# Kernel tuning notes

Measured on AMD Instinct MI355X. Metric: run time of the kernel, lower is better.

The kernel has to match this reference:

```python
import jax, jax.numpy as jnp
import numpy as np


def setup_inputs() -> dict:
    key = jax.random.key(0)
    ks = jax.random.split(key, 8)
    B, N, K, C_in, M, C_add, C_out = 2, 40000, 16, 64, 16, 3, 128
    in_features = (C_in + C_add) * M  # 1072
    input_features = jax.random.normal(ks[0], (B, N, C_in), dtype=jnp.float32)
    neighbor_inds = jax.random.randint(ks[1], (B, N, K), 0, N, dtype=jnp.int64)
    inverse_neighbors = jax.random.randint(ks[2], (B, N * K), 0, N * K, dtype=jnp.int64)
    inverse_k = jax.random.randint(ks[3], (B, N * K), 0, K, dtype=jnp.int64)
    inverse_idx = jax.random.randint(ks[4], (B, N * K), 0, N, dtype=jnp.int64)
    weightnet = jax.random.normal(ks[5], (B, N, K, M), dtype=jnp.float32)
    additional_features = jax.random.normal(ks[6], (B, N, K, C_add), dtype=jnp.float32)
    bound = 1.0 / np.sqrt(in_features)
    kw, kb = jax.random.split(ks[7])
    linear_weight = jax.random.uniform(kw, (C_out, in_features), dtype=jnp.float32, minval=-bound, maxval=bound)
    linear_bias = jax.random.uniform(kb, (C_out,), dtype=jnp.float32, minval=-bound, maxval=bound)
    return {
        "input_features": input_features,
        "neighbor_inds": neighbor_inds,
        "inverse_neighbors": inverse_neighbors,
        "inverse_k": inverse_k,
        "inverse_idx": inverse_idx,
        "weightnet": weightnet,
        "additional_features": additional_features,
        "linear_weight": linear_weight,
        "linear_bias": linear_bias,
    }


def reference(input_features, neighbor_inds, inverse_neighbors, inverse_k, inverse_idx,
              weightnet, additional_features, linear_weight, linear_bias):
    # inverse_* tensors are only used by the custom CUDA backward; unused here.
    B, N, K = neighbor_inds.shape
    # gather neighbor features: [B, N, K, C_in]
    gathered = jnp.take_along_axis(input_features[:, :, None, :],
                                   neighbor_inds[..., None], axis=1)
    # concat extra per-neighbor features -> [B, N, K, C]
    feats = jnp.concatenate([gathered, additional_features], axis=-1)
    # PConv: [B,N,C,K] @ [B,N,K,M] -> [B,N,C,M] -> flatten to [B,N,C*M]
    pconv = jnp.einsum('bnkc,bnkm->bncm', feats, weightnet)
    pconv = pconv.reshape(B, N, -1)
    # fused linear
    out = jnp.einsum('bnf,of->bno', pconv, linear_weight) + linear_bias
    return out
```

## Files before the change

kernel.cpp:

```cpp
#include <hip/hip_runtime.h>
#include <stdint.h>

typedef unsigned short u16;
typedef short short8 __attribute__((ext_vector_type(8)));
typedef float floatx4 __attribute__((ext_vector_type(4)));

#define NPERB   40000
#define NPTS    80000
#define KNBR    16
#define CIN     64
#define MDIM    16
#define CADD    3
#define CF      (CIN + CADD)
#define COUT    128
#define KF      1072
#define KP      1088
#define NKT     34
#define PTSB    16
#define SLAB    65
#define GRB     64
#define PPB     8

__device__ __forceinline__ u16 f2bf(float f) {
    union { float f; unsigned int u; } v; v.f = f;
    unsigned int u = v.u;
    return (u16)((u + 0x7FFFu + ((u >> 16) & 1u)) >> 16);
}
__device__ __forceinline__ short8 pack8(floatx4 x, floatx4 y) {
    union { short8 v; u16 a[8]; } u;
    u.a[0] = f2bf(x[0]); u.a[1] = f2bf(x[1]); u.a[2] = f2bf(x[2]); u.a[3] = f2bf(x[3]);
    u.a[4] = f2bf(y[0]); u.a[5] = f2bf(y[1]); u.a[6] = f2bf(y[2]); u.a[7] = f2bf(y[3]);
    return u.v;
}
__device__ __forceinline__ unsigned swz(unsigned chunk) {
    return chunk ^ ((chunk >> 3) & 7u);
}
__device__ __forceinline__ void gload_lds16(const void* g, void* l) {
    __builtin_amdgcn_global_load_lds(
        (const __attribute__((address_space(1))) void*)g,
        (__attribute__((address_space(3))) void*)l, 16, 0, 0);
}

__global__ void prep_lw_kernel(const float* __restrict__ lw, u16* __restrict__ lwp) {
    int i = blockIdx.x * 256 + threadIdx.x;
    if (i >= COUT * KP) return;
    int o = i / KP, f = i - o * KP;
    lwp[i] = (f < KF) ? f2bf(lw[(size_t)o * KF + f]) : (u16)0;
}

__device__ __forceinline__ void emit_point(
    int lane, float av, const float (&fv)[KNBR], const float* wl,
    u16* __restrict__ dst)
{
    const int em = lane & 15, ec = lane >> 4;
    float ev = 0.f;
#pragma unroll
    for (int k = 0; k < KNBR; k++)
        ev += __shfl(av, k * CADD + ec) * wl[k * MDIM + em];
    if (ec == 3) ev = 0.f;
    dst[1024 + lane] = f2bf(ev);

    floatx4 a0 = 0, a1 = 0, a2 = 0, a3 = 0;
#pragma unroll
    for (int k = 0; k < KNBR; k++) {
        const floatx4* w4 = (const floatx4*)(wl + k * MDIM);
        const float fvk = fv[k];
        a0 += fvk * w4[0]; a1 += fvk * w4[1];
        a2 += fvk * w4[2]; a3 += fvk * w4[3];
    }
    *(short8*)(dst + lane * 16)     = pack8(a0, a1);
    *(short8*)(dst + lane * 16 + 8) = pack8(a2, a3);
}

__global__ __launch_bounds__(256) void pconv_kernel(
    const float* __restrict__ inp,
    const int*   __restrict__ nbr,
    const float* __restrict__ wn,
    const float* __restrict__ addl,
    u16* __restrict__ pc)
{
    __shared__ __align__(16) float Wns[PPB * KNBR * MDIM];

    const int wave = threadIdx.x >> 6;
    const int lane = threadIdx.x & 63;
    const int pbase = blockIdx.x * PPB;
    const float* inpb = inp + ((pbase >= NPERB) ? (size_t)NPERB * CIN : 0);

    const int pr0 = wave * 2;
    const int p0  = __builtin_amdgcn_readfirstlane(pbase + pr0);
    const int p1  = p0 + 1;

    float* wl0 = Wns + pr0 * (KNBR * MDIM);
    float* wl1 = wl0 + KNBR * MDIM;
    gload_lds16(wn + (size_t)p0 * (KNBR * MDIM) + lane * 4, wl0);
    gload_lds16(wn + (size_t)p1 * (KNBR * MDIM) + lane * 4, wl1);

    float av0 = (lane < KNBR * CADD) ? addl[(size_t)p0 * (KNBR * CADD) + lane] : 0.f;
    float av1 = (lane < KNBR * CADD) ? addl[(size_t)p1 * (KNBR * CADD) + lane] : 0.f;

    const int* nb0 = nbr + (size_t)p0 * KNBR;
    const int* nb1 = nbr + (size_t)p1 * KNBR;
    int idx0[KNBR], idx1[KNBR];
#pragma unroll
    for (int k = 0; k < KNBR; k++) idx0[k] = nb0[k];
#pragma unroll
    for (int k = 0; k < KNBR; k++) idx1[k] = nb1[k];

    float fv0[KNBR], fv1[KNBR];
#pragma unroll
    for (int k = 0; k < KNBR; k++) fv0[k] = inpb[(size_t)idx0[k] * CIN + lane];
#pragma unroll
    for (int k = 0; k < KNBR; k++) fv1[k] = inpb[(size_t)idx1[k] * CIN + lane];

    asm volatile("s_waitcnt vmcnt(0)" ::: "memory");
    __builtin_amdgcn_sched_barrier(0);

    emit_point(lane, av0, fv0, wl0, pc + (size_t)p0 * KP);
    emit_point(lane, av1, fv1, wl1, pc + (size_t)p1 * KP);
}

__global__ __launch_bounds__(256) void gemm_kernel(
    const u16* __restrict__ pc,
    const u16* __restrict__ lwp,
    const float* __restrict__ bias,
    float* __restrict__ out)
{
    __shared__ __align__(16) u16 As[4 * 4 * 1024];

    const int wave = threadIdx.x >> 6;
    const int lane = threadIdx.x & 63;
    const int r16 = lane & 15, quad = lane >> 4;
    const int rh = wave >> 1, ch = wave & 1;
    const int row0 = blockIdx.x * GRB + rh * 32;
    const int cb   = ch * 64;

    const int srow = lane >> 2;
    const int sq   = (lane & 3) ^ ((lane >> 3) & 3);
    const u16* aS0 = pc + (size_t)(row0 + srow) * KP + sq * 8;
    const u16* aS1 = pc + (size_t)(row0 + 16 + srow) * KP + sq * 8;
    u16* aD = &As[wave * 4096];

    const unsigned cA0 = (((unsigned)r16 << 2) | ((unsigned)quad ^ ((r16 >> 1) & 3))) << 3;

    const u16* bB0 = lwp + (size_t)(cb + r16) * KP + quad * 8;
    const u16* bB1 = bB0 + (size_t)16 * KP;
    const u16* bB2 = bB0 + (size_t)32 * KP;
    const u16* bB3 = bB0 + (size_t)48 * KP;

    float bv[4];
#pragma unroll
    for (int n = 0; n < 4; n++) bv[n] = bias[cb + n * 16 + r16];
    __builtin_amdgcn_sched_barrier(0);

    floatx4 acc0[4], acc1[4];
#pragma unroll
    for (int n = 0; n < 4; n++) { acc0[n] = 0; acc1[n] = 0; }

    short8 Bq[3][4];

#define STAGE(s) { \
    gload_lds16(aS0 + (s) * 32, aD + ((s) & 3) * 1024); \
    gload_lds16(aS1 + (s) * 32, aD + ((s) & 3) * 1024 + 512); }

#define LOADB(t) { \
    Bq[(t) % 3][0] = *(const short8*)(bB0 + (t) * 32); \
    Bq[(t) % 3][1] = *(const short8*)(bB1 + (t) * 32); \
    Bq[(t) % 3][2] = *(const short8*)(bB2 + (t) * 32); \
    Bq[(t) % 3][3] = *(const short8*)(bB3 + (t) * 32); }

    STAGE(0) STAGE(1) STAGE(2)
    __builtin_amdgcn_sched_barrier(0);
    LOADB(0)
    __builtin_amdgcn_sched_barrier(0);
    LOADB(1)
    __builtin_amdgcn_sched_barrier(0);

#define STEP(kt, N) { \
    if ((kt) + 2 < NKT) { LOADB((kt) + 2) __builtin_amdgcn_sched_barrier(0); } \
    if ((kt) + 3 < NKT) { STAGE((kt) + 3) __builtin_amdgcn_sched_barrier(0); } \
    asm volatile("s_waitcnt vmcnt(" #N ")" ::: "memory"); \
    __builtin_amdgcn_sched_barrier(0); \
    short8 A0 = *(const short8*)(aD + ((kt) & 3) * 1024 + cA0); \
    short8 A1 = *(const short8*)(aD + ((kt) & 3) * 1024 + cA0 + 512); \
    asm volatile("s_waitcnt lgkmcnt(0)" ::: "memory"); \
    __builtin_amdgcn_sched_barrier(0); \
    _Pragma("unroll") \
    for (int n = 0; n < 4; n++) { \
        acc0[n] = __builtin_amdgcn_mfma_f32_16x16x32_bf16(A0, Bq[(kt) % 3][n], acc0[n], 0, 0, 0); \
        acc1[n] = __builtin_amdgcn_mfma_f32_16x16x32_bf16(A1, Bq[(kt) % 3][n], acc1[n], 0, 0, 0); \
    } }

    STEP(0, 10)  STEP(1, 12)  STEP(2, 14)  STEP(3, 14)  STEP(4, 14)
    STEP(5, 14)  STEP(6, 14)  STEP(7, 14)  STEP(8, 14)  STEP(9, 14)
    STEP(10, 14) STEP(11, 14) STEP(12, 14) STEP(13, 14) STEP(14, 14)
    STEP(15, 14) STEP(16, 14) STEP(17, 14) STEP(18, 14) STEP(19, 14)
    STEP(20, 14) STEP(21, 14) STEP(22, 14) STEP(23, 14) STEP(24, 14)
    STEP(25, 14) STEP(26, 14) STEP(27, 14) STEP(28, 14) STEP(29, 14)
    STEP(30, 14) STEP(31, 12) STEP(32, 6)  STEP(33, 0)

#undef STEP
#undef LOADB
#undef STAGE

#pragma unroll
    for (int r = 0; r < 4; r++) {
        {
            const size_t row = (size_t)(row0 + quad * 4 + r) * COUT;
#pragma unroll
            for (int n = 0; n < 4; n++)
                out[row + cb + n * 16 + r16] = acc0[n][r] + bv[n];
        }
        {
            const size_t row = (size_t)(row0 + 16 + quad * 4 + r) * COUT;
#pragma unroll
            for (int n = 0; n < 4; n++)
                out[row + cb + n * 16 + r16] = acc1[n][r] + bv[n];
        }
    }
}

__device__ __forceinline__ void compute_point(
    int pr, int lane, float av, const float (&fv)[KNBR],
    const float* wl, u16* Apc)
{
    const int em = lane & 15, ec = lane >> 4;
    float ev = 0.f;
#pragma unroll
    for (int k = 0; k < KNBR; k++)
        ev += __shfl(av, k * CADD + ec) * wl[k * MDIM + em];
    if (ec == 3) ev = 0.f;
    {
        unsigned kt   = 32 + (lane >> 5);
        unsigned quad = (lane >> 3) & 3;
        unsigned ch   = kt * SLAB + (unsigned)pr * 4 + quad;
        Apc[swz(ch) * 8 + (lane & 7)] = f2bf(ev);
    }
    floatx4 a0 = 0, a1 = 0, a2 = 0, a3 = 0;
#pragma unroll
    for (int k = 0; k < KNBR; k++) {
        const floatx4* w4 = (const floatx4*)(wl + k * MDIM);
        const float fvk = fv[k];
        a0 += fvk * w4[0]; a1 += fvk * w4[1];
        a2 += fvk * w4[2]; a3 += fvk * w4[3];
    }
    {
        unsigned kt = lane >> 1, qb = (lane & 1) * 2;
        unsigned ch = kt * SLAB + (unsigned)pr * 4 + qb;
        *(short8*)&Apc[swz(ch) * 8]     = pack8(a0, a1);
        *(short8*)&Apc[swz(ch + 1) * 8] = pack8(a2, a3);
    }
}

__global__ __launch_bounds__(512, 6) void fused_kernel(
    const float* __restrict__ inp, const int* __restrict__ nbr,
    const float* __restrict__ wn, const float* __restrict__ addl,
    const u16* __restrict__ lwp, const float* __restrict__ bias,
    float* __restrict__ out)
{
    __shared__ __align__(16) u16   Apc[(NKT * SLAB + 8) * 8];
    __shared__ __align__(16) float Wns[PTSB * KNBR * MDIM];

    const int wave = threadIdx.x >> 6;
    const int lane = threadIdx.x & 63;
    const int pbase = blockIdx.x * PTSB;
    const float* inpb = inp + ((pbase >= NPERB) ? (size_t)NPERB * CIN : 0);

    const int pr0 = wave * 2;
    const int p0  = __builtin_amdgcn_readfirstlane(pbase + pr0);
    const int p1  = p0 + 1;

    float* wl0 = Wns + pr0 * (KNBR * MDIM);
    float* wl1 = wl0 + KNBR * MDIM;
    gload_lds16(wn + (size_t)p0 * (KNBR * MDIM) + lane * 4, wl0);
    gload_lds16(wn + (size_t)p1 * (KNBR * MDIM) + lane * 4, wl1);

    float av0 = (lane < KNBR * CADD) ? addl[(size_t)p0 * (KNBR * CADD) + lane] : 0.f;
    float av1 = (lane < KNBR * CADD) ? addl[(size_t)p1 * (KNBR * CADD) + lane] : 0.f;

    const int* nb0 = nbr + (size_t)p0 * KNBR;
    const int* nb1 = nbr + (size_t)p1 * KNBR;
    int idx0[KNBR], idx1[KNBR];
#pragma unroll
    for (int k = 0; k < KNBR; k++) idx0[k] = nb0[k];
#pragma unroll
    for (int k = 0; k < KNBR; k++) idx1[k] = nb1[k];

    float fv0[KNBR], fv1[KNBR];
#pragma unroll
    for (int k = 0; k < KNBR; k++) fv0[k] = inpb[(size_t)idx0[k] * CIN + lane];
#pragma unroll
    for (int k = 0; k < KNBR; k++) fv1[k] = inpb[(size_t)idx1[k] * CIN + lane];

    asm volatile("s_waitcnt vmcnt(0)" ::: "memory");
    __builtin_amdgcn_sched_barrier(0);

    compute_point(pr0,     lane, av0, fv0, wl0, Apc);
    compute_point(pr0 + 1, lane, av1, fv1, wl1, Apc);

    const int r16 = lane & 15, quad = lane >> 4;
    const int c0 = wave * 16;
    const u16* Bp = lwp + (size_t)(c0 + r16) * KP + quad * 8;
    const unsigned abase = (unsigned)r16 * 4 + quad;
    const float bv = bias[c0 + r16];

    __syncthreads();

    floatx4 acc = 0;
#pragma unroll 2
    for (int kt = 0; kt < NKT; kt++) {
        short8 A = *(const short8*)&Apc[swz((unsigned)kt * SLAB + abase) * 8];
        short8 B = *(const short8*)(Bp + kt * 32);
        acc = __builtin_amdgcn_mfma_f32_16x16x32_bf16(A, B, acc, 0, 0, 0);
    }

#pragma unroll
    for (int r = 0; r < 4; r++) {
        const size_t row = (size_t)(pbase + quad * 4 + r) * COUT;
        out[row + c0 + r16] = acc[r] + bv;
    }
}

__global__ __launch_bounds__(256) void fused_fallback_kernel(
    const float* __restrict__ inp, const int* __restrict__ nbr,
    const float* __restrict__ wn, const float* __restrict__ addl,
    const float* __restrict__ lw, const float* __restrict__ bias,
    float* __restrict__ out)
{
    const int p = blockIdx.x;
    const int b = p / NPERB;
    const int tid = threadIdx.x;
    __shared__ float sf[KNBR * CF];
    __shared__ float sw[KNBR * MDIM];
    __shared__ float sp[KF];

    sw[tid] = wn[(size_t)p * (KNBR * MDIM) + tid];
    for (int i = tid; i < KNBR * CIN; i += 256) {
        int k = i >> 6, c = i & 63;
        int idx = nbr[(size_t)p * KNBR + k];
        sf[k * CF + c] = inp[((size_t)b * NPERB + idx) * CIN + c];
    }
    if (tid < KNBR * CADD) {
        int k = tid / CADD, c = tid - k * CADD;
        sf[k * CF + CIN + c] = addl[(size_t)p * (KNBR * CADD) + tid];
    }
    __syncthreads();
    for (int f = tid; f < KF; f += 256) {
        int c = f >> 4, m = f & 15;
        float s = 0;
#pragma unroll
        for (int k = 0; k < KNBR; k++) s += sf[k * CF + c] * sw[k * MDIM + m];
        sp[f] = s;
    }
    __syncthreads();
    const int o = tid >> 1, h = tid & 1;
    float s = 0;
    for (int f = h * (KF / 2); f < (h + 1) * (KF / 2); f++)
        s += sp[f] * lw[(size_t)o * KF + f];
    s += __shfl_xor(s, 1);
    if (h == 0) out[(size_t)p * COUT + o] = s + bias[o];
}

extern "C" void kernel_launch(void* const* d_in, const int* in_sizes, int n_in,
                              void* d_out, int out_size, void* d_ws, size_t ws_size,
                              hipStream_t stream) {
    const float* inp  = (const float*)d_in[0];
    const int*   nbr  = (const int*)d_in[1];
    const float* wn   = (const float*)d_in[5];
    const float* addl = (const float*)d_in[6];
    const float* lw   = (const float*)d_in[7];
    const float* bias = (const float*)d_in[8];
    float* out = (float*)d_out;

    const size_t lw_bytes = (size_t)COUT * KP * sizeof(u16);
    const size_t pc_bytes = (size_t)NPTS * KP * sizeof(u16);

    if (ws_size >= lw_bytes + pc_bytes) {
        u16* lwp = (u16*)d_ws;
        u16* pcw = lwp + (size_t)COUT * KP;
        prep_lw_kernel<<<(COUT * KP + 255) / 256, 256, 0, stream>>>(lw, lwp);
        pconv_kernel<<<NPTS / PPB, 256, 0, stream>>>(inp, nbr, wn, addl, pcw);
        gemm_kernel<<<NPTS / GRB, 256, 0, stream>>>(pcw, lwp, bias, out);
    } else if (ws_size >= lw_bytes) {
        u16* lwp = (u16*)d_ws;
        prep_lw_kernel<<<(COUT * KP + 255) / 256, 256, 0, stream>>>(lw, lwp);
        fused_kernel<<<NPTS / PTSB, 512, 0, stream>>>(inp, nbr, wn, addl, lwp, bias, out);
    } else {
        fused_fallback_kernel<<<NPTS, 256, 0, stream>>>(inp, nbr, wn, addl, lw, bias, out);
    }
}
```

Baseline: 335.3 us.

## Preload whole 32-row A tile into padded LDS, halve GEMM block rows

The GEMM kernel now handles 32 rows per block instead of 64. Rather than streaming A k-slices through a 4-stage ring, it loads the entire 32x1088 bf16 tile into LDS up front with padded rows (2192 bytes), then double-buffers A fragment reads from LDS against the MFMA loop. The intent is to remove per-step global-to-LDS staging and its waits, and to double the grid for more parallelism. In exchange each block uses about 70KB of LDS, which lowers occupancy and halves reuse of the B fragments. The workspace layout is also swapped so the pconv buffer comes first.

```diff
diff --git a/kernel.cpp b/kernel.cpp
--- a/kernel.cpp
+++ b/kernel.cpp
@@ -18,8 +18,9 @@
 #define NKT     34
 #define PTSB    16
 #define SLAB    65
-#define GRB     64
+#define GRB     32
 #define PPB     8
+#define LROWB   2192
 
 __device__ __forceinline__ u16 f2bf(float f) {
     union { float f; unsigned int u; } v; v.f = f;
@@ -125,22 +126,27 @@
     const float* __restrict__ bias,
     float* __restrict__ out)
 {
-    __shared__ __align__(16) u16 As[4 * 4 * 1024];
+    __shared__ __align__(16) u16 As[69 * 512];
 
     const int wave = threadIdx.x >> 6;
     const int lane = threadIdx.x & 63;
     const int r16 = lane & 15, quad = lane >> 4;
     const int rh = wave >> 1, ch = wave & 1;
-    const int row0 = blockIdx.x * GRB + rh * 32;
-    const int cb   = ch * 64;
-
-    const int srow = lane >> 2;
-    const int sq   = (lane & 3) ^ ((lane >> 3) & 3);
-    const u16* aS0 = pc + (size_t)(row0 + srow) * KP + sq * 8;
-    const u16* aS1 = pc + (size_t)(row0 + 16 + srow) * KP + sq * 8;
-    u16* aD = &As[wave * 4096];
-
-    const unsigned cA0 = (((unsigned)r16 << 2) | ((unsigned)quad ^ ((r16 >> 1) & 3))) << 3;
+    const int row0 = blockIdx.x * GRB;
+    const int cb = ch * 64;
+
+    const char* srcb = (const char*)pc + (size_t)row0 * (KP * 2);
+#pragma unroll
+    for (int j = 0; j < 18; j++) {
+        const int w = j * 4 + wave;
+        if (w < 69) {
+            const unsigned d   = (unsigned)w * 1024u + (unsigned)lane * 16u;
+            const unsigned row = d / (unsigned)LROWB;
+            const unsigned col = d - row * (unsigned)LROWB;
+            gload_lds16(srcb + (size_t)row * 2176u + col,
+                        (char*)As + (size_t)w * 1024u);
+        }
+    }
 
     const u16* bB0 = lwp + (size_t)(cb + r16) * KP + quad * 8;
     const u16* bB1 = bB0 + (size_t)16 * KP;
@@ -150,17 +156,15 @@
     float bv[4];
 #pragma unroll
     for (int n = 0; n < 4; n++) bv[n] = bias[cb + n * 16 + r16];
-    __builtin_amdgcn_sched_barrier(0);
-
-    floatx4 acc0[4], acc1[4];
-#pragma unroll
-    for (int n = 0; n < 4; n++) { acc0[n] = 0; acc1[n] = 0; }
+
+    const u16* aRd = As + (size_t)(rh * 16 + r16) * (LROWB / 2) + quad * 8;
+
+    floatx4 acc[4];
+#pragma unroll
+    for (int n = 0; n < 4; n++) acc[n] = 0;
 
     short8 Bq[3][4];
-
-#define STAGE(s) { \
-    gload_lds16(aS0 + (s) * 32, aD + ((s) & 3) * 1024); \
-    gload_lds16(aS1 + (s) * 32, aD + ((s) & 3) * 1024 + 512); }
+    short8 AR0, AR1;
 
 #define LOADB(t) { \
     Bq[(t) % 3][0] = *(const short8*)(bB0 + (t) * 32); \
@@ -168,54 +172,46 @@
     Bq[(t) % 3][2] = *(const short8*)(bB2 + (t) * 32); \
     Bq[(t) % 3][3] = *(const short8*)(bB3 + (t) * 32); }
 
-    STAGE(0) STAGE(1) STAGE(2)
-    __builtin_amdgcn_sched_barrier(0);
     LOADB(0)
     __builtin_amdgcn_sched_barrier(0);
     LOADB(1)
     __builtin_amdgcn_sched_barrier(0);
 
-#define STEP(kt, N) { \
+    asm volatile("s_waitcnt vmcnt(8)" ::: "memory");
+    __syncthreads();
+    AR0 = *(const short8*)aRd;
+
+#define STEP(kt, NV, NL) { \
     if ((kt) + 2 < NKT) { LOADB((kt) + 2) __builtin_amdgcn_sched_barrier(0); } \
-    if ((kt) + 3 < NKT) { STAGE((kt) + 3) __builtin_amdgcn_sched_barrier(0); } \
-    asm volatile("s_waitcnt vmcnt(" #N ")" ::: "memory"); \
+    if ((kt) + 1 < NKT) { \
+        if ((((kt) + 1) & 1) == 0) AR0 = *(const short8*)(aRd + ((kt) + 1) * 32); \
+        else                       AR1 = *(const short8*)(aRd + ((kt) + 1) * 32); \
+    } \
     __builtin_amdgcn_sched_barrier(0); \
-    short8 A0 = *(const short8*)(aD + ((kt) & 3) * 1024 + cA0); \
-    short8 A1 = *(const short8*)(aD + ((kt) & 3) * 1024 + cA0 + 512); \
-    asm volatile("s_waitcnt lgkmcnt(0)" ::: "memory"); \
+    asm volatile("s_waitcnt vmcnt(" #NV ") lgkmcnt(" #NL ")" ::: "memory"); \
     __builtin_amdgcn_sched_barrier(0); \
     _Pragma("unroll") \
-    for (int n = 0; n < 4; n++) { \
-        acc0[n] = __builtin_amdgcn_mfma_f32_16x16x32_bf16(A0, Bq[(kt) % 3][n], acc0[n], 0, 0, 0); \
-        acc1[n] = __builtin_amdgcn_mfma_f32_16x16x32_bf16(A1, Bq[(kt) % 3][n], acc1[n], 0, 0, 0); \
-    } }
-
-    STEP(0, 10)  STEP(1, 12)  STEP(2, 14)  STEP(3, 14)  STEP(4, 14)
-    STEP(5, 14)  STEP(6, 14)  STEP(7, 14)  STEP(8, 14)  STEP(9, 14)
-    STEP(10, 14) STEP(11, 14) STEP(12, 14) STEP(13, 14) STEP(14, 14)
-    STEP(15, 14) STEP(16, 14) STEP(17, 14) STEP(18, 14) STEP(19, 14)
-    STEP(20, 14) STEP(21, 14) STEP(22, 14) STEP(23, 14) STEP(24, 14)
-    STEP(25, 14) STEP(26, 14) STEP(27, 14) STEP(28, 14) STEP(29, 14)
-    STEP(30, 14) STEP(31, 12) STEP(32, 6)  STEP(33, 0)
+    for (int n = 0; n < 4; n++) \
+        acc[n] = __builtin_amdgcn_mfma_f32_16x16x32_bf16( \
+            (((kt) & 1) == 0) ? AR0 : AR1, Bq[(kt) % 3][n], acc[n], 0, 0, 0); }
+
+    STEP(0, 8, 1)  STEP(1, 8, 1)  STEP(2, 8, 1)  STEP(3, 8, 1)  STEP(4, 8, 1)
+    STEP(5, 8, 1)  STEP(6, 8, 1)  STEP(7, 8, 1)  STEP(8, 8, 1)  STEP(9, 8, 1)
+    STEP(10, 8, 1) STEP(11, 8, 1) STEP(12, 8, 1) STEP(13, 8, 1) STEP(14, 8, 1)
+    STEP(15, 8, 1) STEP(16, 8, 1) STEP(17, 8, 1) STEP(18, 8, 1) STEP(19, 8, 1)
+    STEP(20, 8, 1) STEP(21, 8, 1) STEP(22, 8, 1) STEP(23, 8, 1) STEP(24, 8, 1)
+    STEP(25, 8, 1) STEP(26, 8, 1) STEP(27, 8, 1) STEP(28, 8, 1) STEP(29, 8, 1)
+    STEP(30, 8, 1) STEP(31, 8, 1) STEP(32, 4, 1) STEP(33, 0, 0)
 
 #undef STEP
 #undef LOADB
-#undef STAGE
 
 #pragma unroll
     for (int r = 0; r < 4; r++) {
-        {
-            const size_t row = (size_t)(row0 + quad * 4 + r) * COUT;
-#pragma unroll
-            for (int n = 0; n < 4; n++)
-                out[row + cb + n * 16 + r16] = acc0[n][r] + bv[n];
-        }
-        {
-            const size_t row = (size_t)(row0 + 16 + quad * 4 + r) * COUT;
-#pragma unroll
-            for (int n = 0; n < 4; n++)
-                out[row + cb + n * 16 + r16] = acc1[n][r] + bv[n];
-        }
+        const size_t row = (size_t)(row0 + rh * 16 + quad * 4 + r) * COUT;
+#pragma unroll
+        for (int n = 0; n < 4; n++)
+            out[row + cb + n * 16 + r16] = acc[n][r] + bv[n];
     }
 }
 
@@ -375,8 +371,8 @@
     const size_t pc_bytes = (size_t)NPTS * KP * sizeof(u16);
 
     if (ws_size >= lw_bytes + pc_bytes) {
-        u16* lwp = (u16*)d_ws;
-        u16* pcw = lwp + (size_t)COUT * KP;
+        u16* pcw = (u16*)d_ws;
+        u16* lwp = pcw + (size_t)NPTS * KP;
         prep_lw_kernel<<<(COUT * KP + 255) / 256, 256, 0, stream>>>(lw, lwp);
         pconv_kernel<<<NPTS / PPB, 256, 0, stream>>>(inp, nbr, wn, addl, pcw);
         gemm_kernel<<<NPTS / GRB, 256, 0, stream>>>(pcw, lwp, bias, out);
```

New measurement: 383.6 us. 1.14x slower.
